# Optimization experiments

Measured on AMD Instinct MI355X. Metric: run time of the kernel, lower is better.

Reference implementation:

```python
import jax, jax.numpy as jnp
import numpy as np

HEADDIM = 128
CHUNK = 256


def _ssd_scan(x, dt, A, B, C, chunk):
    # x: (b,l,h,p)  dt: (b,l,h)  A: (h,)  B,C: (b,l,n)  (single group g=1 shared by all heads)
    b, l, h, p = x.shape
    n = B.shape[-1]
    nc = l // chunk
    dA = dt * A  # (b,l,h)
    xc = x.reshape(b, nc, chunk, h, p)
    dtc = dt.reshape(b, nc, chunk, h)
    dAc = dA.reshape(b, nc, chunk, h)
    Bc = B.reshape(b, nc, chunk, n)
    Cc = C.reshape(b, nc, chunk, n)
    cs = jnp.cumsum(dAc, axis=2)  # (b,nc,c,h) cumulative log-decay within chunk
    # intra-chunk quadratic part
    CB = jnp.einsum('bjin,bjkn->bjik', Cc, Bc)  # (b,nc,c,c)
    decay = jnp.exp(cs[:, :, :, None, :] - cs[:, :, None, :, :])  # (b,nc,i,k,h)
    mask = jnp.tril(jnp.ones((chunk, chunk), dtype=bool))
    decay = jnp.where(mask[None, None, :, :, None], decay, 0.0)
    y_intra = jnp.einsum('bjik,bjikh,bjkh,bjkhp->bjihp', CB, decay, dtc, xc)
    # per-chunk end states
    decay_states = jnp.exp(cs[:, :, -1:, :] - cs)  # (b,nc,c,h)
    states = jnp.einsum('bjkh,bjkh,bjkn,bjkhp->bjhnp', decay_states, dtc, Bc, xc)
    # recurrence across chunks: h_j = exp(sum dA_j) * h_{j-1} + states_j
    chunk_decay = jnp.exp(cs[:, :, -1, :])  # (b,nc,h)
    def step(carry, inp):
        s, d = inp
        new = carry * d[:, :, None, None] + s
        return new, carry  # emit state BEFORE this chunk
    init = jnp.zeros((b, h, n, p), x.dtype)
    _, prev = jax.lax.scan(step, init,
                           (states.transpose(1, 0, 2, 3, 4), chunk_decay.transpose(1, 0, 2)))
    prev = prev.transpose(1, 0, 2, 3, 4)  # (b,nc,h,n,p)
    y_inter = jnp.einsum('bjih,bjin,bjhnp->bjihp', jnp.exp(cs), Cc, prev)
    return (y_intra + y_inter).reshape(b, l, h, p)


def setup_inputs() -> dict:
    key = jax.random.key(0)
    k1, k2, k3, k4 = jax.random.split(key, 4)
    b, l, d_inner, nheads, d_state = 2, 4096, 2048, 16, 256
    x = jax.random.normal(k1, (b, l, d_inner), dtype=jnp.float32)
    BC = jax.random.normal(k2, (b, l, 2 * d_state), dtype=jnp.float32) * 0.1
    dt = jax.random.normal(k3, (b, l, 2 * nheads), dtype=jnp.float32) - 3.0
    A_log = jnp.zeros((nheads,), dtype=jnp.float32)
    D = jnp.ones((nheads,), dtype=jnp.float32)
    W_fcD = jax.random.normal(k4, (nheads, d_inner), dtype=jnp.float32) * 0.02
    return {"x": x, "BC": BC, "dt": dt, "A_log": A_log, "D": D, "W_fcD": W_fcD}


def reference(x, BC, dt, A_log, D, W_fcD):
    b, l, dim = x.shape
    h = A_log.shape[0]
    p = HEADDIM
    d_state = BC.shape[-1] // 2
    A = -jnp.exp(A_log)
    # bidirectional: concat forward stream with time-flipped backward stream along batch
    dt2 = jnp.concatenate((dt[:, :, :h], jnp.flip(dt[:, :, h:], axis=1)), axis=0)
    dt2 = jax.nn.softplus(dt2)
    x_og = x
    x2 = jnp.concatenate((x, jnp.flip(x, axis=1)), axis=0)
    BC2 = jnp.concatenate((BC, jnp.flip(BC, axis=1)), axis=0)
    B, C = BC2[..., :d_state], BC2[..., d_state:]
    y = _ssd_scan(x2.reshape(2 * b, l, h, p), dt2, A, B, C, CHUNK)
    y = y.reshape(2 * b, l, dim)
    y = jnp.roll(y, shift=1, axis=1).at[:, 0, :].set(0.0)
    y_fw, y_bw = y[:b], jnp.flip(y[b:], axis=1)
    gate = x_og @ W_fcD.T + D  # (b,l,h)
    y = y_fw + y_bw + x_og * jnp.repeat(gate, p, axis=-1)
    return y
```

## Files before the change

### kernel.cpp

```cpp
#include <hip/hip_runtime.h>
#include <stdint.h>

#define NB 2
#define SL 4096
#define NH 16
#define HD 128
#define DS 256
#define CK 256
#define NCH 16
#define NSQ 4
#define DI 2048

typedef unsigned short u16;
typedef unsigned int u32;
typedef __attribute__((ext_vector_type(8))) __bf16 bf16x8;
typedef __attribute__((ext_vector_type(4))) float f32x4;

__device__ __forceinline__ int tor(int dir, int t) { return dir ? (SL - 1 - t) : t; }

__device__ __forceinline__ u16 f2bf(float f) {
  u32 u = __float_as_uint(f);
  u = u + 0x7fffu + ((u >> 16) & 1u);
  return (u16)(u >> 16);
}
__device__ __forceinline__ float bf2f(u16 s) {
  return __uint_as_float(((u32)s) << 16);
}

__device__ __forceinline__ void gl_lds16(const u16* g, u16* l) {
  __builtin_amdgcn_global_load_lds((const __attribute__((address_space(1))) u32*)g,
                                   (__attribute__((address_space(3))) u32*)l, 16, 0, 0);
}

__device__ __forceinline__ void cfence() { asm volatile("" ::: "memory"); }
__device__ __forceinline__ void spin() { __builtin_amdgcn_sched_barrier(0); }

__device__ __forceinline__ void stage_tile(const u16* __restrict__ src, u16* lds,
                                           int lane, int w, int k0) {
  int sgrow = lane >> 2, sc = lane & 3;
  int r0 = w << 5;
  int ra = r0 + sgrow, rb = ra + 16;
  int kqa = (sc ^ ((ra >> 1) & 3)) << 3;
  int kqb = (sc ^ ((rb >> 1) & 3)) << 3;
  gl_lds16(src + (size_t)ra * 256 + k0 + kqa, lds + r0 * 32);
  gl_lds16(src + (size_t)rb * 256 + k0 + kqb, lds + (r0 + 16) * 32);
}

__device__ __forceinline__ void stage_half(const u16* __restrict__ src, u16* lds,
                                           int lane, int w, int k0) {
  int row = (w << 4) + (lane >> 2);
  int sc = lane & 3;
  int kq = (sc ^ ((row >> 1) & 3)) << 3;
  gl_lds16(src + (size_t)row * 256 + k0 + kq, lds + (w << 4) * 32);
}

__device__ __forceinline__ bf16x8 frag(const u16* lds, int base_row, int m, int quad) {
  int row = base_row + m;
  return *(const bf16x8*)&lds[row * 32 + ((quad ^ ((row >> 1) & 3)) << 3)];
}

__device__ __forceinline__ void mfma16(const u16* As, const u16* Bs, int wi, int wp,
                                       int m, int quad, f32x4 acc[4][4]) {
  bf16x8 af[4], bv[4];
#pragma unroll
  for (int r = 0; r < 4; ++r) af[r] = frag(As, wi + (r << 4), m, quad);
#pragma unroll
  for (int c = 0; c < 4; ++c) bv[c] = frag(Bs, wp + (c << 4), m, quad);
#pragma unroll
  for (int r = 0; r < 4; ++r)
#pragma unroll
    for (int c = 0; c < 4; ++c)
      acc[r][c] = __builtin_amdgcn_mfma_f32_16x16x32_bf16(af[r], bv[c], acc[r][c], 0, 0, 0);
}

__global__ __launch_bounds__(256) void kprep(const float* __restrict__ dt,
                                             const float* __restrict__ A_log,
                                             float* __restrict__ csb,
                                             float* __restrict__ dtvb,
                                             float* __restrict__ cdecb) {
  int blk = blockIdx.x;
  int h = blk & 15, sj = blk >> 4;
  int s = sj >> 4, j = sj & 15;
  int b = s & 1, dir = s >> 1;
  int i = threadIdx.x;
  int to = tor(dir, j * CK + i);
  __shared__ float sbuf[CK];
  float a = -expf(A_log[h]);
  float raw = dt[((size_t)(b * SL + to)) * (2 * NH) + dir * NH + h];
  float sp = (raw > 20.f) ? raw : log1pf(expf(raw));
  sbuf[i] = sp * a;
  __syncthreads();
  for (int off = 1; off < CK; off <<= 1) {
    float v = (i >= off) ? sbuf[i - off] : 0.f;
    __syncthreads();
    sbuf[i] += v;
    __syncthreads();
  }
  float csv = sbuf[i];
  size_t base = ((size_t)sj * NH + h) * CK;
  csb[base + i] = csv;
  dtvb[base + i] = sp;
  if (i == CK - 1) cdecb[sj * NH + h] = expf(csv);
}

__global__ __launch_bounds__(256) void kcast(const float* __restrict__ BC,
                                             u16* __restrict__ Bbf,
                                             u16* __restrict__ Cbf) {
  int blk = blockIdx.x;
  int s = blk >> 9, tg = blk & 511;
  int b = s & 1, dir = s >> 1;
  int tid = threadIdx.x;
  int rr = tid >> 6, q = tid & 63;
  int isC = q >> 5, qq = q & 31;
#pragma unroll
  for (int it = 0; it < 2; ++it) {
    int t = tg * 8 + it * 4 + rr;
    int tsrc = tor(dir, t);
    const float* src = BC + ((size_t)(b * SL + tsrc)) * (2 * DS) + q * 8;
    float4 v0 = ((const float4*)src)[0];
    float4 v1 = ((const float4*)src)[1];
    uint4 wv;
    wv.x = (u32)f2bf(v0.x) | ((u32)f2bf(v0.y) << 16);
    wv.y = (u32)f2bf(v0.z) | ((u32)f2bf(v0.w) << 16);
    wv.z = (u32)f2bf(v1.x) | ((u32)f2bf(v1.y) << 16);
    wv.w = (u32)f2bf(v1.z) | ((u32)f2bf(v1.w) << 16);
    u16* dstb = (isC ? Cbf : Bbf) + ((size_t)s * SL + t) * DS + qq * 8;
    *(uint4*)dstb = wv;
  }
}

__global__ __launch_bounds__(256) void ktransB(const u16* __restrict__ Bbf,
                                               u16* __restrict__ BbfT) {
  int blk = blockIdx.x;
  int kslice = blk & 3, sj = blk >> 2;
  int k0 = kslice << 6;
  int s = sj >> 4, j = sj & 15;
  __shared__ u16 T[64 * 264];
  int tid = threadIdx.x;
  const u16* src = Bbf + ((size_t)s * SL + j * CK) * DS;
  u16* dst = BbfT + (size_t)sj * DS * CK;
  int kr = tid >> 2, part = (tid & 3) * 64;
  {
    const uint4* gs = (const uint4*)(src + (size_t)(k0 + kr) * DS + part);
    uint4* tb = (uint4*)&T[kr * 264 + part];
#pragma unroll
    for (int q = 0; q < 8; ++q) tb[q] = gs[q];
  }
  __syncthreads();
  int n = tid;
  u16 col[64];
#pragma unroll
  for (int kq = 0; kq < 64; ++kq) col[kq] = T[kq * 264 + n];
  uint4* ds_ = (uint4*)(dst + (size_t)n * CK + k0);
#pragma unroll
  for (int q = 0; q < 8; ++q) {
    uint4 wv;
    wv.x = (u32)col[q * 8 + 0] | ((u32)col[q * 8 + 1] << 16);
    wv.y = (u32)col[q * 8 + 2] | ((u32)col[q * 8 + 3] << 16);
    wv.z = (u32)col[q * 8 + 4] | ((u32)col[q * 8 + 5] << 16);
    wv.w = (u32)col[q * 8 + 6] | ((u32)col[q * 8 + 7] << 16);
    ds_[q] = wv;
  }
}

__global__ __launch_bounds__(256) void kxsT(const float* __restrict__ xg,
                                            const float* __restrict__ csb,
                                            const float* __restrict__ dtvb,
                                            u16* __restrict__ xsT) {
  int inst = blockIdx.x;
  int h = inst & 15, sj = inst >> 4;
  int s = sj >> 4, j = sj & 15;
  int b = s & 1, dir = s >> 1;
  int tid = threadIdx.x;
  __shared__ u16 Ls[128 * 40];
  size_t cbase = ((size_t)sj * NH + h) * CK;
  u16* dst = xsT + (size_t)inst * (128 * 256);
  int kk = tid >> 3;
  int pg = (tid & 7) * 16;
  int p2 = tid >> 1, half = tid & 1;
  for (int k0 = 0; k0 < CK; k0 += 32) {
    int kglob = k0 + kk;
    float sc_ = expf(-csb[cbase + kglob]) * dtvb[cbase + kglob];
    int t = tor(dir, j * CK + kglob);
    const float* src = xg + ((size_t)(b * SL + t)) * DI + h * HD + pg;
    float4 v0 = ((const float4*)src)[0];
    float4 v1 = ((const float4*)src)[1];
    float4 v2 = ((const float4*)src)[2];
    float4 v3 = ((const float4*)src)[3];
    float vv[16] = {v0.x, v0.y, v0.z, v0.w, v1.x, v1.y, v1.z, v1.w,
                    v2.x, v2.y, v2.z, v2.w, v3.x, v3.y, v3.z, v3.w};
    __syncthreads();
#pragma unroll
    for (int q = 0; q < 16; ++q) Ls[(pg + q) * 40 + kk] = f2bf(vv[q] * sc_);
    __syncthreads();
    uint4 w0 = *(const uint4*)&Ls[p2 * 40 + half * 16];
    uint4 w1 = *(const uint4*)&Ls[p2 * 40 + half * 16 + 8];
    *(uint4*)&dst[(size_t)p2 * 256 + k0 + half * 16] = w0;
    *(uint4*)&dst[(size_t)p2 * 256 + k0 + half * 16 + 8] = w1;
  }
}

__global__ __launch_bounds__(256) void kcb(const u16* __restrict__ Cbf,
                                           const u16* __restrict__ Bbf,
                                           u16* __restrict__ CBm) {
  int blk = blockIdx.x;
  int tri = blk % 3;
  int sj = blk / 3;
  int it0 = tri ? 128 : 0;
  int kt0 = (tri == 2) ? 128 : 0;
  int s = sj >> 4, j = sj & 15;
  __shared__ u16 As[2][128 * 32];
  __shared__ u16 Bs[2][128 * 32];
  int tid = threadIdx.x;
  int w = tid >> 6, lane = tid & 63;
  int wi = (w >> 1) << 6, wp = (w & 1) << 6;
  int m = lane & 15, quad = lane >> 4;
  const u16* Ab = Cbf + ((size_t)s * SL + j * CK + it0) * DS;
  const u16* Bb = Bbf + ((size_t)s * SL + j * CK + kt0) * DS;
  f32x4 zini = {0.f, 0.f, 0.f, 0.f};
  f32x4 acc[4][4];
#pragma unroll
  for (int r = 0; r < 4; ++r)
#pragma unroll
    for (int c = 0; c < 4; ++c) acc[r][c] = zini;
  stage_tile(Ab, As[0], lane, w, 0);
  stage_tile(Bb, Bs[0], lane, w, 0);
  int cur = 0;
  for (int ks = 0; ks < 8; ++ks) {
    if (ks + 1 < 8) {
      int k1 = (ks + 1) << 5;
      stage_tile(Ab, As[cur ^ 1], lane, w, k1);
      stage_tile(Bb, Bs[cur ^ 1], lane, w, k1);
      cfence();
      asm volatile("s_waitcnt vmcnt(4)" ::: "memory");
    } else {
      cfence();
      asm volatile("s_waitcnt vmcnt(0)" ::: "memory");
    }
    spin();
    __builtin_amdgcn_s_barrier();
    spin();
    mfma16(As[cur], Bs[cur], wi, wp, m, quad, acc);
    spin();
    __builtin_amdgcn_s_barrier();
    spin();
    cur ^= 1;
  }
  int diag = (it0 == kt0);
  u16* dst = CBm + ((size_t)sj * CK + it0) * CK + kt0;
#pragma unroll
  for (int r = 0; r < 4; ++r)
#pragma unroll
    for (int rg = 0; rg < 4; ++rg) {
      int irow = wi + (r << 4) + (quad << 2) + rg;
#pragma unroll
      for (int c = 0; c < 4; ++c) {
        int kcol = wp + (c << 4) + m;
        float v = acc[r][c][rg];
        if (diag && kcol > irow) v = 0.f;
        dst[(size_t)irow * CK + kcol] = f2bf(v);
      }
    }
}

__global__ __launch_bounds__(512) void kstates(const u16* __restrict__ xsT,
                                               const u16* __restrict__ BbfT,
                                               const float* __restrict__ cdecb,
                                               u16* __restrict__ prevT) {
  int inst = blockIdx.x;
  int h = inst & 15, sj = inst >> 4;
  __shared__ u16 As[2][128 * 32];
  __shared__ u16 Bs[2][256 * 32];
  int tid = threadIdx.x;
  int w = tid >> 6, lane = tid & 63;
  int wi = (w >> 2) << 6;
  int wp = (w & 3) << 6;
  int m = lane & 15, quad = lane >> 4;
  const u16* Ab = xsT + (size_t)inst * (128 * 256);
  const u16* Bb = BbfT + (size_t)sj * DS * CK;
  f32x4 zini = {0.f, 0.f, 0.f, 0.f};
  f32x4 acc[4][4];
#pragma unroll
  for (int r = 0; r < 4; ++r)
#pragma unroll
    for (int c = 0; c < 4; ++c) acc[r][c] = zini;
  stage_half(Ab, As[0], lane, w, 0);
  stage_tile(Bb, Bs[0], lane, w, 0);
  int cur = 0;
  for (int ks = 0; ks < 8; ++ks) {
    if (ks + 1 < 8) {
      int k1 = (ks + 1) << 5;
      stage_half(Ab, As[cur ^ 1], lane, w, k1);
      stage_tile(Bb, Bs[cur ^ 1], lane, w, k1);
      cfence();
      asm volatile("s_waitcnt vmcnt(3)" ::: "memory");
    } else {
      cfence();
      asm volatile("s_waitcnt vmcnt(0)" ::: "memory");
    }
    spin();
    __builtin_amdgcn_s_barrier();
    spin();
    mfma16(As[cur], Bs[cur], wi, wp, m, quad, acc);
    spin();
    __builtin_amdgcn_s_barrier();
    spin();
    cur ^= 1;
  }
  float scale = cdecb[sj * NH + h];
  u16* dst = prevT + (size_t)inst * (128 * 256);
#pragma unroll
  for (int r = 0; r < 4; ++r)
#pragma unroll
    for (int rg = 0; rg < 4; ++rg) {
      int prow = wi + (r << 4) + (quad << 2) + rg;
#pragma unroll
      for (int c = 0; c < 4; ++c) {
        int ncol = wp + (c << 4) + m;
        dst[(size_t)prow * 256 + ncol] = f2bf(acc[r][c][rg] * scale);
      }
    }
}

__global__ __launch_bounds__(256) void kscan(u16* __restrict__ prevT,
                                             const float* __restrict__ cdecb) {
  int g = blockIdx.x * 256 + threadIdx.x;
  int n = g & 255;
  int p = (g >> 8) & 127;
  int h = (g >> 15) & 15;
  int s = g >> 19;
  size_t base = (((size_t)(s * 256 + h) * 128) + p) * 256 + n;
  const size_t stride = (size_t)NH * 128 * 256;
  float carry = 0.f;
  for (int j = 0; j < NCH; ++j) {
    size_t idx = base + (size_t)j * stride;
    float sv = bf2f(prevT[idx]);
    prevT[idx] = f2bf(carry);
    carry = carry * cdecb[(s * NCH + j) * NH + h] + sv;
  }
}

__global__ __launch_bounds__(512) void ky(const u16* __restrict__ CBm,
                                          const u16* __restrict__ Cbf,
                                          const u16* __restrict__ xsT,
                                          const u16* __restrict__ prevT,
                                          const float* __restrict__ csb,
                                          u16* __restrict__ ytmpb) {
  int inst = blockIdx.x;
  int h = inst & 15, sj = inst >> 4;
  int s = sj >> 4, j = sj & 15;
  __shared__ u16 As[2][256 * 32];
  __shared__ u16 Bs[2][128 * 32];
  int tid = threadIdx.x;
  int w = tid >> 6, lane = tid & 63;
  int wi = (w >> 1) << 6;
  int wp = (w & 1) << 6;
  int m = lane & 15, quad = lane >> 4;

  const u16* Ai = CBm + (size_t)sj * CK * CK;
  const u16* Ae = Cbf + ((size_t)s * SL + j * CK) * DS;
  const u16* Bi = xsT + (size_t)inst * (128 * 256);
  const u16* Be = prevT + (size_t)inst * (128 * 256);

  f32x4 zini = {0.f, 0.f, 0.f, 0.f};
  f32x4 acc[4][4];
#pragma unroll
  for (int r = 0; r < 4; ++r)
#pragma unroll
    for (int c = 0; c < 4; ++c) acc[r][c] = zini;

  stage_tile(Ai, As[0], lane, w, 0);
  stage_half(Bi, Bs[0], lane, w, 0);
  int cur = 0;
  for (int ks = 0; ks < 16; ++ks) {
    if (ks + 1 < 16) {
      int ksn = ks + 1;
      int intran = ksn < 8;
      int k1 = (intran ? ksn : ksn - 8) << 5;
      stage_tile(intran ? Ai : Ae, As[cur ^ 1], lane, w, k1);
      stage_half(intran ? Bi : Be, Bs[cur ^ 1], lane, w, k1);
      cfence();
      asm volatile("s_waitcnt vmcnt(3)" ::: "memory");
    } else {
      cfence();
      asm volatile("s_waitcnt vmcnt(0)" ::: "memory");
    }
    spin();
    __builtin_amdgcn_s_barrier();
    spin();
    if (ks >= 8 || ks < 4 || wi >= 128)
      mfma16(As[cur], Bs[cur], wi, wp, m, quad, acc);
    spin();
    __builtin_amdgcn_s_barrier();
    spin();
    cur ^= 1;
  }
  const float* csrow = csb + ((size_t)sj * NH + h) * CK;
  u16* yb = ytmpb + ((size_t)s * SL + j * CK) * DI + h * HD;
#pragma unroll
  for (int r = 0; r < 4; ++r)
#pragma unroll
    for (int rg = 0; rg < 4; ++rg) {
      int irow = wi + (r << 4) + (quad << 2) + rg;
      float esc = expf(csrow[irow]);
#pragma unroll
      for (int c = 0; c < 4; ++c) {
        int pcol = wp + (c << 4) + m;
        yb[(size_t)irow * DI + pcol] = f2bf(acc[r][c][rg] * esc);
      }
    }
}

__global__ __launch_bounds__(256) void kgate(const float* __restrict__ xg,
                                             const float* __restrict__ Wg,
                                             const float* __restrict__ Dg,
                                             float* __restrict__ gates) {
  int bid = blockIdx.x;
  int b = bid >> 8;
  int t0 = (bid & 255) << 4;
  __shared__ float Wl[16 * 256];
  int tid = threadIdx.x;
  int w = tid >> 6, lane = tid & 63;
  int c4 = lane << 2;

  float acc[4][16];
#pragma unroll
  for (int r = 0; r < 4; ++r)
#pragma unroll
    for (int h = 0; h < 16; ++h) acc[r][h] = 0.f;

  for (int i = 0; i < 8; ++i) {
    __syncthreads();
#pragma unroll
    for (int q = 0; q < 4; ++q) {
      int idx = q * 256 + tid;
      int h = idx >> 6;
      int c = (idx & 63) << 2;
      *(float4*)&Wl[h * 256 + c] = *(const float4*)&Wg[(size_t)h * DI + i * 256 + c];
    }
    __syncthreads();
    float4 Wf[16];
#pragma unroll
    for (int h = 0; h < 16; ++h) Wf[h] = *(const float4*)&Wl[h * 256 + c4];
#pragma unroll
    for (int r = 0; r < 4; ++r) {
      int t = t0 + (w << 2) + r;
      float4 xv = *(const float4*)&xg[((size_t)(b * SL + t)) * DI + i * 256 + c4];
#pragma unroll
      for (int h = 0; h < 16; ++h)
        acc[r][h] += xv.x * Wf[h].x + xv.y * Wf[h].y + xv.z * Wf[h].z + xv.w * Wf[h].w;
    }
  }
#pragma unroll
  for (int r = 0; r < 4; ++r)
#pragma unroll
    for (int h = 0; h < 16; ++h) {
      float v = acc[r][h];
      v += __shfl_xor(v, 32);
      v += __shfl_xor(v, 16);
      v += __shfl_xor(v, 8);
      v += __shfl_xor(v, 4);
      v += __shfl_xor(v, 2);
      v += __shfl_xor(v, 1);
      acc[r][h] = v;
    }
  if (lane == 0) {
#pragma unroll
    for (int r = 0; r < 4; ++r) {
      int t = t0 + (w << 2) + r;
      float* gdst = gates + ((size_t)(b * SL + t)) * NH;
#pragma unroll
      for (int h = 0; h < 16; ++h) gdst[h] = acc[r][h] + Dg[h];
    }
  }
}

__device__ __forceinline__ void unpk8(uint4 u, float* o) {
  o[0] = __uint_as_float(u.x << 16); o[1] = __uint_as_float(u.x & 0xffff0000u);
  o[2] = __uint_as_float(u.y << 16); o[3] = __uint_as_float(u.y & 0xffff0000u);
  o[4] = __uint_as_float(u.z << 16); o[5] = __uint_as_float(u.z & 0xffff0000u);
  o[6] = __uint_as_float(u.w << 16); o[7] = __uint_as_float(u.w & 0xffff0000u);
}

__global__ __launch_bounds__(256) void kstream(const float* __restrict__ xg,
                                               const float* __restrict__ gates,
                                               const u16* __restrict__ ytmpb,
                                               float* __restrict__ out) {
  int bid = blockIdx.x;
  int b = bid >> 10;
  int t0 = (bid & 1023) << 2;
  int tid = threadIdx.x;
  int d0 = tid << 3;
  int h8 = tid >> 4;
  const u16* fwbase = ytmpb + (size_t)b * SL * DI + d0;
  const u16* bwbase = ytmpb + (size_t)(2 + b) * SL * DI + d0;
#pragma unroll
  for (int r = 0; r < 4; ++r) {
    int t = t0 + r;
    size_t rowb = ((size_t)(b * SL + t)) * DI + d0;
    float4 x0 = *(const float4*)&xg[rowb];
    float4 x1 = *(const float4*)&xg[rowb + 4];
    float fy[8] = {0.f, 0.f, 0.f, 0.f, 0.f, 0.f, 0.f, 0.f};
    float by[8] = {0.f, 0.f, 0.f, 0.f, 0.f, 0.f, 0.f, 0.f};
    if (t > 0) unpk8(*(const uint4*)(fwbase + (size_t)(t - 1) * DI), fy);
    if (t < SL - 1) unpk8(*(const uint4*)(bwbase + (size_t)(SL - 2 - t) * DI), by);
    float g = gates[((size_t)(b * SL + t)) * NH + h8];
    float4 o0, o1;
    o0.x = fy[0] + by[0] + x0.x * g;
    o0.y = fy[1] + by[1] + x0.y * g;
    o0.z = fy[2] + by[2] + x0.z * g;
    o0.w = fy[3] + by[3] + x0.w * g;
    o1.x = fy[4] + by[4] + x1.x * g;
    o1.y = fy[5] + by[5] + x1.y * g;
    o1.z = fy[6] + by[6] + x1.z * g;
    o1.w = fy[7] + by[7] + x1.w * g;
    *(float4*)&out[rowb] = o0;
    *(float4*)&out[rowb + 4] = o1;
  }
}

extern "C" void kernel_launch(void* const* d_in, const int* in_sizes, int n_in,
                              void* d_out, int out_size, void* d_ws, size_t ws_size,
                              hipStream_t stream) {
  (void)in_sizes; (void)n_in; (void)out_size; (void)ws_size;
  const float* x     = (const float*)d_in[0];
  const float* BC    = (const float*)d_in[1];
  const float* dt    = (const float*)d_in[2];
  const float* A_log = (const float*)d_in[3];
  const float* Dg    = (const float*)d_in[4];
  const float* W     = (const float*)d_in[5];
  float* out = (float*)d_out;

  char* p = (char*)d_ws;
  float* cs    = (float*)p; p += (size_t)NSQ * NCH * NH * CK * 4;
  float* dtv   = (float*)p; p += (size_t)NSQ * NCH * NH * CK * 4;
  float* cdec  = (float*)p; p += (size_t)NSQ * NCH * NH * 4;
  float* gates = (float*)p; p += (size_t)NB * SL * NH * 4;
  u16* Bbf    = (u16*)p;    p += (size_t)NSQ * SL * DS * 2;
  u16* Cbf    = (u16*)p;    p += (size_t)NSQ * SL * DS * 2;
  u16* BbfT   = (u16*)p;    p += (size_t)NSQ * NCH * DS * CK * 2;
  u16* CBm    = (u16*)p;    p += (size_t)NSQ * NCH * CK * CK * 2;
  u16* xsT    = (u16*)p;    p += (size_t)NSQ * NCH * NH * HD * CK * 2;
  u16* prevT  = (u16*)p;    p += (size_t)NSQ * NCH * NH * HD * DS * 2;
  u16* ytmpb  = (u16*)p;    p += (size_t)NSQ * SL * DI * 2;

  hipLaunchKernelGGL(kgate,   dim3(NB * SL / 16),        dim3(256), 0, stream, x, W, Dg, gates);
  hipLaunchKernelGGL(kprep,   dim3(NSQ * NCH * NH),      dim3(CK),  0, stream, dt, A_log, cs, dtv, cdec);
  hipLaunchKernelGGL(kcast,   dim3(NSQ * SL / 8),        dim3(256), 0, stream, BC, Bbf, Cbf);
  hipLaunchKernelGGL(ktransB, dim3(NSQ * NCH * 4),       dim3(256), 0, stream, Bbf, BbfT);
  hipLaunchKernelGGL(kxsT,    dim3(NSQ * NCH * NH),      dim3(256), 0, stream, x, cs, dtv, xsT);
  hipLaunchKernelGGL(kcb,     dim3(NSQ * NCH * 3),       dim3(256), 0, stream, Cbf, Bbf, CBm);
  hipLaunchKernelGGL(kstates, dim3(NSQ * NCH * NH),      dim3(512), 0, stream, xsT, BbfT, cdec, prevT);
  hipLaunchKernelGGL(kscan,   dim3(NSQ * NH * HD * DS / 256), dim3(256), 0, stream, prevT, cdec);
  hipLaunchKernelGGL(ky,      dim3(NSQ * NCH * NH),      dim3(512), 0, stream, CBm, Cbf, xsT, prevT, cs, ytmpb);
  hipLaunchKernelGGL(kstream, dim3(NB * SL / 4),         dim3(256), 0, stream, x, gates, ytmpb, out);
}
```

Before: 361.0 us.

## Triple-buffer GEMM staging, remap block IDs across XCDs, raise MFMA priority

The kstates and ky GEMM loops move from double to triple buffering in shared memory, issuing loads two k-steps ahead with adjusted vmcnt waits to hide more global load latency. Block IDs in kcb, kstates and ky are permuted so that consecutive logical tiles land on the same XCD (bid&7 stride), aiming to improve L2 locality for shared operands. s_setprio raises wave priority around the MFMA section. The extra LDS buffers reduce occupancy, and the remap assumes the grid sizes are exactly 8x the divisor used.

Measured after the change: 372.5 us. 1.03x slower.

```diff
diff --git a/kernel.cpp b/kernel.cpp
--- a/kernel.cpp
+++ b/kernel.cpp
@@ -203,9 +203,10 @@
 __global__ __launch_bounds__(256) void kcb(const u16* __restrict__ Cbf,
                                            const u16* __restrict__ Bbf,
                                            u16* __restrict__ CBm) {
-  int blk = blockIdx.x;
-  int tri = blk % 3;
-  int sj = blk / 3;
+  int bid = blockIdx.x;
+  int g = ((bid & 7) * 24) + (bid >> 3);
+  int tri = g % 3;
+  int sj = g / 3;
   int it0 = tri ? 128 : 0;
   int kt0 = (tri == 2) ? 128 : 0;
   int s = sj >> 4, j = sj & 15;
@@ -240,7 +241,9 @@
     spin();
     __builtin_amdgcn_s_barrier();
     spin();
+    __builtin_amdgcn_s_setprio(1);
     mfma16(As[cur], Bs[cur], wi, wp, m, quad, acc);
+    __builtin_amdgcn_s_setprio(0);
     spin();
     __builtin_amdgcn_s_barrier();
     spin();
@@ -267,10 +270,11 @@
                                                const u16* __restrict__ BbfT,
                                                const float* __restrict__ cdecb,
                                                u16* __restrict__ prevT) {
-  int inst = blockIdx.x;
+  int bid = blockIdx.x;
+  int inst = ((bid & 7) << 7) + (bid >> 3);
   int h = inst & 15, sj = inst >> 4;
-  __shared__ u16 As[2][128 * 32];
-  __shared__ u16 Bs[2][256 * 32];
+  __shared__ u16 As[3][128 * 32];
+  __shared__ u16 Bs[3][256 * 32];
   int tid = threadIdx.x;
   int w = tid >> 6, lane = tid & 63;
   int wi = (w >> 2) << 6;
@@ -286,12 +290,18 @@
     for (int c = 0; c < 4; ++c) acc[r][c] = zini;
   stage_half(Ab, As[0], lane, w, 0);
   stage_tile(Bb, Bs[0], lane, w, 0);
+  stage_half(Ab, As[1], lane, w, 32);
+  stage_tile(Bb, Bs[1], lane, w, 32);
   int cur = 0;
   for (int ks = 0; ks < 8; ++ks) {
-    if (ks + 1 < 8) {
-      int k1 = (ks + 1) << 5;
-      stage_half(Ab, As[cur ^ 1], lane, w, k1);
-      stage_tile(Bb, Bs[cur ^ 1], lane, w, k1);
+    if (ks + 2 < 8) {
+      int nb = cur + 2; if (nb >= 3) nb -= 3;
+      int k2 = (ks + 2) << 5;
+      stage_half(Ab, As[nb], lane, w, k2);
+      stage_tile(Bb, Bs[nb], lane, w, k2);
+      cfence();
+      asm volatile("s_waitcnt vmcnt(6)" ::: "memory");
+    } else if (ks == 6) {
       cfence();
       asm volatile("s_waitcnt vmcnt(3)" ::: "memory");
     } else {
@@ -301,11 +311,13 @@
     spin();
     __builtin_amdgcn_s_barrier();
     spin();
+    __builtin_amdgcn_s_setprio(1);
     mfma16(As[cur], Bs[cur], wi, wp, m, quad, acc);
+    __builtin_amdgcn_s_setprio(0);
     spin();
     __builtin_amdgcn_s_barrier();
     spin();
-    cur ^= 1;
+    cur = (cur == 2) ? 0 : cur + 1;
   }
   float scale = cdecb[sj * NH + h];
   u16* dst = prevT + (size_t)inst * (128 * 256);
@@ -346,11 +358,12 @@
                                           const u16* __restrict__ prevT,
                                           const float* __restrict__ csb,
                                           u16* __restrict__ ytmpb) {
-  int inst = blockIdx.x;
+  int bid = blockIdx.x;
+  int inst = ((bid & 7) << 7) + (bid >> 3);
   int h = inst & 15, sj = inst >> 4;
   int s = sj >> 4, j = sj & 15;
-  __shared__ u16 As[2][256 * 32];
-  __shared__ u16 Bs[2][128 * 32];
+  __shared__ u16 As[3][256 * 32];
+  __shared__ u16 Bs[3][128 * 32];
   int tid = threadIdx.x;
   int w = tid >> 6, lane = tid & 63;
   int wi = (w >> 1) << 6;
@@ -371,14 +384,20 @@
 
   stage_tile(Ai, As[0], lane, w, 0);
   stage_half(Bi, Bs[0], lane, w, 0);
+  stage_tile(Ai, As[1], lane, w, 32);
+  stage_half(Bi, Bs[1], lane, w, 32);
   int cur = 0;
   for (int ks = 0; ks < 16; ++ks) {
-    if (ks + 1 < 16) {
-      int ksn = ks + 1;
+    if (ks + 2 < 16) {
+      int ksn = ks + 2;
       int intran = ksn < 8;
-      int k1 = (intran ? ksn : ksn - 8) << 5;
-      stage_tile(intran ? Ai : Ae, As[cur ^ 1], lane, w, k1);
-      stage_half(intran ? Bi : Be, Bs[cur ^ 1], lane, w, k1);
+      int k2 = (intran ? ksn : ksn - 8) << 5;
+      int nb = cur + 2; if (nb >= 3) nb -= 3;
+      stage_tile(intran ? Ai : Ae, As[nb], lane, w, k2);
+      stage_half(intran ? Bi : Be, Bs[nb], lane, w, k2);
+      cfence();
+      asm volatile("s_waitcnt vmcnt(6)" ::: "memory");
+    } else if (ks == 14) {
       cfence();
       asm volatile("s_waitcnt vmcnt(3)" ::: "memory");
     } else {
@@ -388,12 +407,14 @@
     spin();
     __builtin_amdgcn_s_barrier();
     spin();
+    __builtin_amdgcn_s_setprio(1);
     if (ks >= 8 || ks < 4 || wi >= 128)
       mfma16(As[cur], Bs[cur], wi, wp, m, quad, acc);
+    __builtin_amdgcn_s_setprio(0);
     spin();
     __builtin_amdgcn_s_barrier();
     spin();
-    cur ^= 1;
+    cur = (cur == 2) ? 0 : cur + 1;
   }
   const float* csrow = csb + ((size_t)sj * NH + h) * CK;
   u16* yb = ytmpb + ((size_t)s * SL + j * CK) * DI + h * HD;
```
